# Kernel tuning notes

Hardware: AMD Instinct MI355X
Metric: run time of the kernel (lower is better)

## Reference

```python
import jax, jax.numpy as jnp
import numpy as np

DIM = 2048
NUM_HEADS = 16
HEAD_DIM = DIM // NUM_HEADS  # 128
LC = HEAD_DIM // 2           # 64 complex pairs per head
B, S = 2, 2048
EPS = 1e-6


def setup_inputs() -> dict:
    key = jax.random.key(0)
    ks = jax.random.split(key, 12)
    x = jax.random.normal(ks[0], (B, S, DIM), dtype=jnp.float32)
    # freqs: unit-modulus complex rotations stored as (cos, sin), shape [S,1,LC,2]
    theta = jax.random.uniform(ks[1], (S, 1, LC), dtype=jnp.float32) * (2.0 * np.pi)
    freqs = jnp.stack([jnp.cos(theta), jnp.sin(theta)], axis=-1)
    scale = 0.02
    wq = jax.random.normal(ks[2], (DIM, DIM), dtype=jnp.float32) * scale
    bq = jnp.zeros((DIM,), dtype=jnp.float32)
    wk = jax.random.normal(ks[3], (DIM, DIM), dtype=jnp.float32) * scale
    bk = jnp.zeros((DIM,), dtype=jnp.float32)
    wv = jax.random.normal(ks[4], (DIM, DIM), dtype=jnp.float32) * scale
    bv = jnp.zeros((DIM,), dtype=jnp.float32)
    wo = jax.random.normal(ks[5], (DIM, DIM), dtype=jnp.float32) * scale
    bo = jnp.zeros((DIM,), dtype=jnp.float32)
    gq = jnp.ones((DIM,), dtype=jnp.float32)   # RMSNorm weight for q
    gk = jnp.ones((DIM,), dtype=jnp.float32)   # RMSNorm weight for k
    return {"x": x, "freqs": freqs, "wq": wq, "bq": bq, "wk": wk, "bk": bk,
            "wv": wv, "bv": bv, "wo": wo, "bo": bo, "gq": gq, "gk": gk}


def _rms_norm(x, g):
    xf = x.astype(jnp.float32)
    y = xf * jax.lax.rsqrt(jnp.mean(xf * xf, axis=-1, keepdims=True) + EPS)
    return y.astype(x.dtype) * g


def _rope_apply(x, freqs):
    # x: [B,S,D] -> complex pairs [B,S,H,LC,2]; freqs: [S,1,LC,2] (cos,sin)
    b, s, _ = x.shape
    xp = x.astype(jnp.float32).reshape(b, s, NUM_HEADS, LC, 2)
    xr, xi = xp[..., 0], xp[..., 1]
    cr = freqs[None, :, :, :, 0]  # [1,S,1,LC]
    ci = freqs[None, :, :, :, 1]
    out_r = xr * cr - xi * ci
    out_i = xr * ci + xi * cr
    out = jnp.stack([out_r, out_i], axis=-1).reshape(b, s, DIM)
    return out.astype(x.dtype)


def _attention(q, k, v):
    # q,k,v: [B,S,D] -> multihead SDPA -> [B,S,D]
    b, s, _ = q.shape
    qh = q.reshape(b, s, NUM_HEADS, HEAD_DIM).transpose(0, 2, 1, 3)
    kh = k.reshape(b, s, NUM_HEADS, HEAD_DIM).transpose(0, 2, 1, 3)
    vh = v.reshape(b, s, NUM_HEADS, HEAD_DIM).transpose(0, 2, 1, 3)
    scale = 1.0 / np.sqrt(HEAD_DIM).astype(np.float32)
    scores = jnp.einsum('bhqd,bhkd->bhqk', qh, kh) * scale
    probs = jax.nn.softmax(scores, axis=-1)
    out = jnp.einsum('bhqk,bhkd->bhqd', probs, vh)
    return out.transpose(0, 2, 1, 3).reshape(b, s, DIM)


def reference(x, freqs, wq, bq, wk, bk, wv, bv, wo, bo, gq, gk):
    q = _rms_norm(x @ wq.T + bq, gq)
    k = _rms_norm(x @ wk.T + bk, gk)
    v = x @ wv.T + bv
    q = _rope_apply(q, freqs)
    k = _rope_apply(k, freqs)
    attn = _attention(q, k, v)
    return attn @ wo.T + bo
```

## Files before the change

### kernel.cpp

```cpp
#include <hip/hip_runtime.h>
#include <cstdint>

typedef __bf16 bf16;
typedef __bf16 bf16x8 __attribute__((ext_vector_type(8)));
typedef __bf16 bf16x4 __attribute__((ext_vector_type(4)));
typedef float f32x4 __attribute__((ext_vector_type(4)));

#define DIMN 2048
#define SEQ  2048
#define NH   16
#define HD   128

__device__ __forceinline__ void gld_lds16(const bf16* g, bf16* l) {
    __builtin_amdgcn_global_load_lds(
        (const __attribute__((address_space(1))) void*)g,
        (__attribute__((address_space(3))) void*)l,
        16, 0, 0);
}

__global__ __launch_bounds__(256) void cast_all(
    const float* __restrict__ x,
    const float* __restrict__ wq, const float* __restrict__ wk,
    const float* __restrict__ wv, const float* __restrict__ wo,
    bf16* __restrict__ xb,
    bf16* __restrict__ wqb, bf16* __restrict__ wkb,
    bf16* __restrict__ wvb, bf16* __restrict__ wob)
{
    int id = blockIdx.x;
    const float* src; bf16* dst; int i;
    if (id < 8192) { src = x; dst = xb; i = id * 256 + threadIdx.x; }
    else {
        id -= 8192;
        int w = id >> 12; id &= 4095;
        src = (w == 0) ? wq : (w == 1) ? wk : (w == 2) ? wv : wo;
        dst = (w == 0) ? wqb : (w == 1) ? wkb : (w == 2) ? wvb : wob;
        i = id * 256 + threadIdx.x;
    }
    float4 v = ((const float4*)src)[i];
    bf16x4 o;
    o[0] = (bf16)v.x; o[1] = (bf16)v.y; o[2] = (bf16)v.z; o[3] = (bf16)v.w;
    ((bf16x4*)dst)[i] = o;
}

template<int OUT_F32>
__global__ __launch_bounds__(256) void gemm_bt(
    const bf16* __restrict__ A,
    const bf16* __restrict__ Bw0, const bf16* __restrict__ Bw1, const bf16* __restrict__ Bw2,
    const float* __restrict__ bias0, const float* __restrict__ bias1, const float* __restrict__ bias2,
    void* __restrict__ C0, void* __restrict__ C1, void* __restrict__ C2)
{
    const int K = DIMN, N = DIMN;
    const int vtm = (!OUT_F32) && (blockIdx.z == 2);
    const bf16* Ap; const bf16* Bp; const float* bias; void* Cout;
    if (blockIdx.z == 0)      { Ap = A;   Bp = Bw0; bias = bias0; Cout = C0; }
    else if (blockIdx.z == 1) { Ap = A;   Bp = Bw1; bias = bias1; Cout = C1; }
    else                      { Ap = Bw2; Bp = A;   bias = bias2; Cout = C2; }

    __shared__ __attribute__((aligned(16))) bf16 As[128 * 64];
    __shared__ __attribute__((aligned(16))) bf16 Bs[128 * 64];

    const int t    = threadIdx.x;
    const int lane = t & 63, wave = t >> 6;
    const int l15  = lane & 15, quad = lane >> 4;
    const int wm   = (wave >> 1) * 64, wn = (wave & 1) * 64;
    const long bm = vtm ? (long)blockIdx.x * 128 : (long)blockIdx.y * 128;
    const long bn = vtm ? (long)blockIdx.y * 128 : (long)blockIdx.x * 128;

    const bf16* agp[4]; const bf16* bgp[4]; bf16* asd[4]; bf16* bsd[4];
#pragma unroll
    for (int it = 0; it < 4; it++) {
        int fs  = it * 256 + t;
        int row = fs >> 3;
        int gs  = (fs & 7) ^ (row & 7);
        agp[it] = Ap + (bm + row) * (long)K + gs * 8;
        bgp[it] = Bp + (bn + row) * (long)K + gs * 8;
        asd[it] = As + fs * 8;
        bsd[it] = Bs + fs * 8;
    }
    const int swl = l15 & 7;

    f32x4 acc[4][4] = {};

    for (int k0 = 0; k0 < K; k0 += 64) {
#pragma unroll
        for (int it = 0; it < 4; it++) {
            gld_lds16(agp[it] + k0, asd[it]);
            gld_lds16(bgp[it] + k0, bsd[it]);
        }
        __syncthreads();

#pragma unroll
        for (int ks2 = 0; ks2 < 2; ks2++) {
            const int sw = ((ks2 * 4 + quad) ^ swl) * 8;
            bf16x8 af[4], bfr[4];
#pragma unroll
            for (int i = 0; i < 4; i++)
                af[i] = *(const bf16x8*)(As + (wm + i * 16 + l15) * 64 + sw);
#pragma unroll
            for (int j = 0; j < 4; j++)
                bfr[j] = *(const bf16x8*)(Bs + (wn + j * 16 + l15) * 64 + sw);
#pragma unroll
            for (int i = 0; i < 4; i++)
#pragma unroll
                for (int j = 0; j < 4; j++)
                    acc[i][j] = __builtin_amdgcn_mfma_f32_16x16x32_bf16(af[i], bfr[j], acc[i][j], 0, 0, 0);
        }
        __syncthreads();
    }

    if (vtm) {
#pragma unroll
        for (int j = 0; j < 4; j++) {
            const long col = bn + wn + j * 16 + l15;
            const long cb = col >> 11, cs = col & (SEQ - 1);
#pragma unroll
            for (int i = 0; i < 4; i++) {
                const long m0 = bm + wm + i * 16 + quad * 4;
#pragma unroll
                for (int r = 0; r < 4; r++)
                    ((bf16*)Cout)[((cb * DIMN + m0 + r) * SEQ) + cs] =
                        (bf16)(acc[i][j][r] + bias[m0 + r]);
            }
        }
    } else {
#pragma unroll
        for (int j = 0; j < 4; j++) {
            const long col = bn + wn + j * 16 + l15;
            const float bv = bias[col];
#pragma unroll
            for (int i = 0; i < 4; i++) {
                const long row0 = bm + wm + i * 16 + quad * 4;
#pragma unroll
                for (int r = 0; r < 4; r++) {
                    float v = acc[i][j][r] + bv;
                    if (OUT_F32) ((float*)Cout)[(row0 + r) * N + col] = v;
                    else         ((bf16*)Cout)[(row0 + r) * N + col] = (bf16)v;
                }
            }
        }
    }
}

__global__ __launch_bounds__(256) void norm_prep(
    bf16* __restrict__ q, bf16* __restrict__ k,
    const float* __restrict__ gq, const float* __restrict__ gk,
    const float* __restrict__ freqs)
{
    const int id = blockIdx.x;
    const int t = threadIdx.x;
    const int qk  = id >> 12;
    const int row = id & 4095;
    bf16* ptr = qk ? k : q;
    const float* g = qk ? gk : gq;
    const float osc = qk ? 1.0f : 0.12753138080219222f;
    const int s = row & (SEQ - 1);
    const int lane = t & 63, wave = t >> 6;

    bf16* base = ptr + (long)row * DIMN + t * 8;
    bf16x8 raw = *(const bf16x8*)base;
    float v[8]; float ss = 0.f;
#pragma unroll
    for (int j = 0; j < 8; j++) { v[j] = (float)raw[j]; ss += v[j] * v[j]; }
#pragma unroll
    for (int off = 32; off; off >>= 1) ss += __shfl_xor(ss, off, 64);
    __shared__ float red[4];
    if (lane == 0) red[wave] = ss;
    __syncthreads();
    float tot = red[0] + red[1] + red[2] + red[3];
    float rn = rsqrtf(tot * (1.0f / DIMN) + 1e-6f);

    const int e0 = t * 8;
    bf16x8 o;
#pragma unroll
    for (int pp = 0; pp < 4; pp++) {
        int e = e0 + pp * 2;
        float xr = v[pp * 2]     * rn * g[e];
        float xi = v[pp * 2 + 1] * rn * g[e + 1];
        int lc = (e >> 1) & 63;
        float cr = freqs[s * 128 + lc * 2];
        float ci = freqs[s * 128 + lc * 2 + 1];
        o[pp * 2]     = (bf16)((xr * cr - xi * ci) * osc);
        o[pp * 2 + 1] = (bf16)((xr * ci + xi * cr) * osc);
    }
    *(bf16x8*)base = o;
}

__global__ __launch_bounds__(512, 2) void attention(
    const bf16* __restrict__ Q, const bf16* __restrict__ Kb,
    const bf16* __restrict__ Vt, bf16* __restrict__ O)
{
    __shared__ __attribute__((aligned(16))) bf16 Ksh[2][64 * 128];
    __shared__ __attribute__((aligned(16))) bf16 Vsh[2][128 * 64];
    __shared__ __attribute__((aligned(16))) bf16 Psh[8][32 * 72];
    __shared__ float Lsh[8][32];

    const int t = threadIdx.x;
    const int lane = t & 63, w = t >> 6;
    const int l15 = lane & 15, quad = lane >> 4;
    const int bh = blockIdx.x, b = bh >> 4, h = bh & 15;
    const int qt = blockIdx.y;
    const long qrow0 = (long)b * SEQ + qt * 256 + w * 32;
    const bf16* qbase = Q  + qrow0 * DIMN + h * HD;
    const bf16* kbase = Kb + (long)b * SEQ * DIMN + h * HD;
    const bf16* vbase = Vt + (long)bh * HD * SEQ;

    bf16x8 qf[2][4];
#pragma unroll
    for (int im = 0; im < 2; im++)
#pragma unroll
        for (int kd = 0; kd < 4; kd++)
            qf[im][kd] = *(const bf16x8*)(qbase + (long)(im * 16 + l15) * DIMN + kd * 32 + quad * 8);

    long koff[2], voff[2];
#pragma unroll
    for (int it = 0; it < 2; it++) {
        int fs = it * 512 + t;
        int kr = fs >> 4, kp = fs & 15;
        koff[it] = (long)kr * DIMN + (kp ^ (kr & 15)) * 8;
        int dr = fs >> 3, vp = fs & 7;
        voff[it] = (long)dr * SEQ + (vp ^ (dr & 7)) * 8;
    }

    f32x4 o_acc[2][8] = {};
    float Lt[2] = {0.f, 0.f};

#pragma unroll
    for (int it = 0; it < 2; it++) {
        gld_lds16(kbase + koff[it], &Ksh[0][(it * 512 + t) * 8]);
        gld_lds16(vbase + voff[it], &Vsh[0][(it * 512 + t) * 8]);
    }
    __syncthreads();

    for (int kt = 0; kt < 32; kt++) {
        const int cur = kt & 1;
        if (kt < 31) {
            const bf16* kg = kbase + (long)((kt + 1) * 64) * DIMN;
            const bf16* vg = vbase + (kt + 1) * 64;
#pragma unroll
            for (int it = 0; it < 2; it++) {
                gld_lds16(kg + koff[it], &Ksh[cur ^ 1][(it * 512 + t) * 8]);
                gld_lds16(vg + voff[it], &Vsh[cur ^ 1][(it * 512 + t) * 8]);
            }
        }
        const bf16* K0 = Ksh[cur];
        const bf16* V0 = Vsh[cur];

        f32x4 st[4][2] = {};
        __builtin_amdgcn_s_setprio(1);
#pragma unroll
        for (int jk = 0; jk < 4; jk++)
#pragma unroll
            for (int kd = 0; kd < 4; kd++) {
                bf16x8 kf = *(const bf16x8*)(K0 + (jk * 16 + l15) * 128 + (((kd * 4 + quad) ^ l15) & 15) * 8);
                st[jk][0] = __builtin_amdgcn_mfma_f32_16x16x32_bf16(kf, qf[0][kd], st[jk][0], 0, 0, 0);
                st[jk][1] = __builtin_amdgcn_mfma_f32_16x16x32_bf16(kf, qf[1][kd], st[jk][1], 0, 0, 0);
            }
        __builtin_amdgcn_s_setprio(0);

#pragma unroll
        for (int im = 0; im < 2; im++) {
            float part = 0.f;
#pragma unroll
            for (int jk = 0; jk < 4; jk++) {
                bf16x4 pk;
#pragma unroll
                for (int r = 0; r < 4; r++) {
                    float e = exp2f(st[jk][im][r]);
                    part += e;
                    pk[r] = (bf16)e;
                }
                *(bf16x4*)(Psh[w] + (im * 16 + l15) * 72 + jk * 16 + quad * 4) = pk;
            }
            Lt[im] += part;
        }

        __builtin_amdgcn_s_setprio(1);
#pragma unroll
        for (int kd2 = 0; kd2 < 2; kd2++) {
            bf16x8 pa[2];
            pa[0] = *(const bf16x8*)(Psh[w] + (l15)      * 72 + kd2 * 32 + quad * 8);
            pa[1] = *(const bf16x8*)(Psh[w] + (16 + l15) * 72 + kd2 * 32 + quad * 8);
#pragma unroll
            for (int dj = 0; dj < 8; dj++) {
                bf16x8 vfr = *(const bf16x8*)(V0 + (dj * 16 + l15) * 64 + (((kd2 * 4 + quad) ^ l15) & 7) * 8);
                o_acc[0][dj] = __builtin_amdgcn_mfma_f32_16x16x32_bf16(pa[0], vfr, o_acc[0][dj], 0, 0, 0);
                o_acc[1][dj] = __builtin_amdgcn_mfma_f32_16x16x32_bf16(pa[1], vfr, o_acc[1][dj], 0, 0, 0);
            }
        }
        __builtin_amdgcn_s_setprio(0);
        __syncthreads();
    }

#pragma unroll
    for (int im = 0; im < 2; im++) {
        Lt[im] += __shfl_xor(Lt[im], 16, 64);
        Lt[im] += __shfl_xor(Lt[im], 32, 64);
    }
    if (quad == 0) { Lsh[w][l15] = Lt[0]; Lsh[w][16 + l15] = Lt[1]; }
    __syncthreads();

#pragma unroll
    for (int im = 0; im < 2; im++)
#pragma unroll
        for (int r = 0; r < 4; r++) {
            float inv = 1.0f / Lsh[w][im * 16 + quad * 4 + r];
            long orow = qrow0 + im * 16 + quad * 4 + r;
#pragma unroll
            for (int dj = 0; dj < 8; dj++)
                O[orow * DIMN + h * HD + dj * 16 + l15] = (bf16)(o_acc[im][dj][r] * inv);
        }
}

extern "C" void kernel_launch(void* const* d_in, const int* in_sizes, int n_in,
                              void* d_out, int out_size, void* d_ws, size_t ws_size,
                              hipStream_t stream) {
    const float* x     = (const float*)d_in[0];
    const float* freqs = (const float*)d_in[1];
    const float* wq    = (const float*)d_in[2];
    const float* bq    = (const float*)d_in[3];
    const float* wk    = (const float*)d_in[4];
    const float* bk    = (const float*)d_in[5];
    const float* wv    = (const float*)d_in[6];
    const float* bv    = (const float*)d_in[7];
    const float* wo    = (const float*)d_in[8];
    const float* bo    = (const float*)d_in[9];
    const float* gq    = (const float*)d_in[10];
    const float* gk    = (const float*)d_in[11];
    float* out = (float*)d_out;

    const size_t MAT  = (size_t)4096 * 2048 * 2;
    const size_t WMAT = (size_t)2048 * 2048 * 2;
    char* p = (char*)d_ws;
    bf16* xb  = (bf16*)p; p += MAT;
    bf16* wqb = (bf16*)p; p += WMAT;
    bf16* wkb = (bf16*)p; p += WMAT;
    bf16* wvb = (bf16*)p; p += WMAT;
    bf16* wob = (bf16*)p; p += WMAT;
    bf16* qb  = (bf16*)p; p += MAT;
    bf16* kb  = (bf16*)p; p += MAT;
    bf16* vt  = (bf16*)p; p += MAT;
    bf16* attn = qb;

    cast_all<<<24576, 256, 0, stream>>>(x, wq, wk, wv, wo, xb, wqb, wkb, wvb, wob);

    gemm_bt<0><<<dim3(16, 32, 3), 256, 0, stream>>>(xb, wqb, wkb, wvb,
                                                    bq, bk, bv, qb, kb, vt);

    norm_prep<<<8192, 256, 0, stream>>>(qb, kb, gq, gk, freqs);
    attention<<<dim3(32, 8), 512, 0, stream>>>(qb, kb, vt, attn);
    gemm_bt<1><<<dim3(16, 32, 1), 256, 0, stream>>>(attn, wob, wob, wob,
                                                    bo, bo, bo, out, out, out);
}
```

Before: 401.9 us.

## Use 32x32 MFMA in attention with register-resident P via permlane swap

```diff
diff --git a/kernel.cpp b/kernel.cpp
--- a/kernel.cpp
+++ b/kernel.cpp
@@ -5,6 +5,7 @@
 typedef __bf16 bf16x8 __attribute__((ext_vector_type(8)));
 typedef __bf16 bf16x4 __attribute__((ext_vector_type(4)));
 typedef float f32x4 __attribute__((ext_vector_type(4)));
+typedef float f32x16 __attribute__((ext_vector_type(16)));
 
 #define DIMN 2048
 #define SEQ  2048
@@ -42,19 +43,12 @@
     ((bf16x4*)dst)[i] = o;
 }
 
-template<int OUT_F32>
+template<int OUT_F32, int VTM>
 __global__ __launch_bounds__(256) void gemm_bt(
-    const bf16* __restrict__ A,
-    const bf16* __restrict__ Bw0, const bf16* __restrict__ Bw1, const bf16* __restrict__ Bw2,
-    const float* __restrict__ bias0, const float* __restrict__ bias1, const float* __restrict__ bias2,
-    void* __restrict__ C0, void* __restrict__ C1, void* __restrict__ C2)
+    const bf16* __restrict__ A, const bf16* __restrict__ Bw,
+    const float* __restrict__ bias, void* __restrict__ Cout)
 {
     const int K = DIMN, N = DIMN;
-    const int vtm = (!OUT_F32) && (blockIdx.z == 2);
-    const bf16* Ap; const bf16* Bp; const float* bias; void* Cout;
-    if (blockIdx.z == 0)      { Ap = A;   Bp = Bw0; bias = bias0; Cout = C0; }
-    else if (blockIdx.z == 1) { Ap = A;   Bp = Bw1; bias = bias1; Cout = C1; }
-    else                      { Ap = Bw2; Bp = A;   bias = bias2; Cout = C2; }
 
     __shared__ __attribute__((aligned(16))) bf16 As[128 * 64];
     __shared__ __attribute__((aligned(16))) bf16 Bs[128 * 64];
@@ -63,8 +57,8 @@
     const int lane = t & 63, wave = t >> 6;
     const int l15  = lane & 15, quad = lane >> 4;
     const int wm   = (wave >> 1) * 64, wn = (wave & 1) * 64;
-    const long bm = vtm ? (long)blockIdx.x * 128 : (long)blockIdx.y * 128;
-    const long bn = vtm ? (long)blockIdx.y * 128 : (long)blockIdx.x * 128;
+    const long bm = VTM ? (long)blockIdx.x * 128 : (long)blockIdx.y * 128;
+    const long bn = VTM ? (long)blockIdx.y * 128 : (long)blockIdx.x * 128;
 
     const bf16* agp[4]; const bf16* bgp[4]; bf16* asd[4]; bf16* bsd[4];
 #pragma unroll
@@ -72,8 +66,8 @@
         int fs  = it * 256 + t;
         int row = fs >> 3;
         int gs  = (fs & 7) ^ (row & 7);
-        agp[it] = Ap + (bm + row) * (long)K + gs * 8;
-        bgp[it] = Bp + (bn + row) * (long)K + gs * 8;
+        agp[it] = A  + (bm + row) * (long)K + gs * 8;
+        bgp[it] = Bw + (bn + row) * (long)K + gs * 8;
         asd[it] = As + fs * 8;
         bsd[it] = Bs + fs * 8;
     }
@@ -108,7 +102,7 @@
         __syncthreads();
     }
 
-    if (vtm) {
+    if (VTM) {
 #pragma unroll
         for (int j = 0; j < 4; j++) {
             const long col = bn + wn + j * 16 + l15;
@@ -191,12 +185,10 @@
 {
     __shared__ __attribute__((aligned(16))) bf16 Ksh[2][64 * 128];
     __shared__ __attribute__((aligned(16))) bf16 Vsh[2][128 * 64];
-    __shared__ __attribute__((aligned(16))) bf16 Psh[8][32 * 72];
-    __shared__ float Lsh[8][32];
 
     const int t = threadIdx.x;
     const int lane = t & 63, w = t >> 6;
-    const int l15 = lane & 15, quad = lane >> 4;
+    const int l31 = lane & 31, hi = lane >> 5;
     const int bh = blockIdx.x, b = bh >> 4, h = bh & 15;
     const int qt = blockIdx.y;
     const long qrow0 = (long)b * SEQ + qt * 256 + w * 32;
@@ -204,12 +196,10 @@
     const bf16* kbase = Kb + (long)b * SEQ * DIMN + h * HD;
     const bf16* vbase = Vt + (long)bh * HD * SEQ;
 
-    bf16x8 qf[2][4];
-#pragma unroll
-    for (int im = 0; im < 2; im++)
-#pragma unroll
-        for (int kd = 0; kd < 4; kd++)
-            qf[im][kd] = *(const bf16x8*)(qbase + (long)(im * 16 + l15) * DIMN + kd * 32 + quad * 8);
+    bf16x8 qf[8];
+#pragma unroll
+    for (int kd = 0; kd < 8; kd++)
+        qf[kd] = *(const bf16x8*)(qbase + (long)l31 * DIMN + kd * 16 + hi * 8);
 
     long koff[2], voff[2];
 #pragma unroll
@@ -221,8 +211,8 @@
         voff[it] = (long)dr * SEQ + (vp ^ (dr & 7)) * 8;
     }
 
-    f32x4 o_acc[2][8] = {};
-    float Lt[2] = {0.f, 0.f};
+    f32x16 o_acc[4] = {};
+    float Lt = 0.f;
 
 #pragma unroll
     for (int it = 0; it < 2; it++) {
@@ -245,69 +235,75 @@
         const bf16* K0 = Ksh[cur];
         const bf16* V0 = Vsh[cur];
 
-        f32x4 st[4][2] = {};
+        f32x16 st0 = {}, st1 = {};
         __builtin_amdgcn_s_setprio(1);
 #pragma unroll
-        for (int jk = 0; jk < 4; jk++)
-#pragma unroll
-            for (int kd = 0; kd < 4; kd++) {
-                bf16x8 kf = *(const bf16x8*)(K0 + (jk * 16 + l15) * 128 + (((kd * 4 + quad) ^ l15) & 15) * 8);
-                st[jk][0] = __builtin_amdgcn_mfma_f32_16x16x32_bf16(kf, qf[0][kd], st[jk][0], 0, 0, 0);
-                st[jk][1] = __builtin_amdgcn_mfma_f32_16x16x32_bf16(kf, qf[1][kd], st[jk][1], 0, 0, 0);
-            }
+        for (int kd = 0; kd < 8; kd++) {
+            const int sg = ((kd * 2 + hi) ^ (lane & 15)) * 8;
+            bf16x8 kf0 = *(const bf16x8*)(K0 + (l31)      * 128 + sg);
+            bf16x8 kf1 = *(const bf16x8*)(K0 + (32 + l31) * 128 + sg);
+            st0 = __builtin_amdgcn_mfma_f32_32x32x16_bf16(kf0, qf[kd], st0, 0, 0, 0);
+            st1 = __builtin_amdgcn_mfma_f32_32x32x16_bf16(kf1, qf[kd], st1, 0, 0, 0);
+        }
         __builtin_amdgcn_s_setprio(0);
 
-#pragma unroll
-        for (int im = 0; im < 2; im++) {
-            float part = 0.f;
-#pragma unroll
-            for (int jk = 0; jk < 4; jk++) {
-                bf16x4 pk;
-#pragma unroll
-                for (int r = 0; r < 4; r++) {
-                    float e = exp2f(st[jk][im][r]);
-                    part += e;
-                    pk[r] = (bf16)e;
-                }
-                *(bf16x4*)(Psh[w] + (im * 16 + l15) * 72 + jk * 16 + quad * 4) = pk;
-            }
-            Lt[im] += part;
-        }
+        float part = 0.f;
+#pragma unroll
+        for (int r = 0; r < 16; r++) {
+            st0[r] = exp2f(st0[r]); part += st0[r];
+            st1[r] = exp2f(st1[r]); part += st1[r];
+        }
+        Lt += part;
 
         __builtin_amdgcn_s_setprio(1);
 #pragma unroll
-        for (int kd2 = 0; kd2 < 2; kd2++) {
-            bf16x8 pa[2];
-            pa[0] = *(const bf16x8*)(Psh[w] + (l15)      * 72 + kd2 * 32 + quad * 8);
-            pa[1] = *(const bf16x8*)(Psh[w] + (16 + l15) * 72 + kd2 * 32 + quad * 8);
-#pragma unroll
-            for (int dj = 0; dj < 8; dj++) {
-                bf16x8 vfr = *(const bf16x8*)(V0 + (dj * 16 + l15) * 64 + (((kd2 * 4 + quad) ^ l15) & 7) * 8);
-                o_acc[0][dj] = __builtin_amdgcn_mfma_f32_16x16x32_bf16(pa[0], vfr, o_acc[0][dj], 0, 0, 0);
-                o_acc[1][dj] = __builtin_amdgcn_mfma_f32_16x16x32_bf16(pa[1], vfr, o_acc[1][dj], 0, 0, 0);
+        for (int k = 0; k < 4; k++) {
+            const int base = 8 * (k & 1);
+            float e0, e1, e2, e3, e4, e5, e6, e7;
+            if (k < 2) {
+                e0 = st0[base]; e1 = st0[base+1]; e2 = st0[base+2]; e3 = st0[base+3];
+                e4 = st0[base+4]; e5 = st0[base+5]; e6 = st0[base+6]; e7 = st0[base+7];
+            } else {
+                e0 = st1[base]; e1 = st1[base+1]; e2 = st1[base+2]; e3 = st1[base+3];
+                e4 = st1[base+4]; e5 = st1[base+5]; e6 = st1[base+6]; e7 = st1[base+7];
+            }
+            uint32_t W0, W1, W2, W3;
+            asm("v_cvt_pk_bf16_f32 %0, %1, %2" : "=v"(W0) : "v"(e0), "v"(e1));
+            asm("v_cvt_pk_bf16_f32 %0, %1, %2" : "=v"(W1) : "v"(e2), "v"(e3));
+            asm("v_cvt_pk_bf16_f32 %0, %1, %2" : "=v"(W2) : "v"(e4), "v"(e5));
+            asm("v_cvt_pk_bf16_f32 %0, %1, %2" : "=v"(W3) : "v"(e6), "v"(e7));
+            asm volatile("v_permlane32_swap_b32 %0, %1" : "+v"(W0), "+v"(W2));
+            asm volatile("v_permlane32_swap_b32 %0, %1" : "+v"(W1), "+v"(W3));
+            union { uint32_t u[4]; bf16x8 v; } pu;
+            pu.u[0] = W0; pu.u[1] = W1; pu.u[2] = W2; pu.u[3] = W3;
+            const bf16x8 pa = pu.v;
+#pragma unroll
+            for (int dj = 0; dj < 4; dj++) {
+                const bf16x8 vfr = *(const bf16x8*)(V0 + (dj * 32 + l31) * 64 +
+                                                    (((2 * k + hi) ^ (lane & 7)) * 8));
+                o_acc[dj] = __builtin_amdgcn_mfma_f32_32x32x16_bf16(pa, vfr, o_acc[dj], 0, 0, 0);
             }
         }
         __builtin_amdgcn_s_setprio(0);
         __syncthreads();
     }
 
-#pragma unroll
-    for (int im = 0; im < 2; im++) {
-        Lt[im] += __shfl_xor(Lt[im], 16, 64);
-        Lt[im] += __shfl_xor(Lt[im], 32, 64);
-    }
-    if (quad == 0) { Lsh[w][l15] = Lt[0]; Lsh[w][16 + l15] = Lt[1]; }
-    __syncthreads();
-
-#pragma unroll
-    for (int im = 0; im < 2; im++)
-#pragma unroll
-        for (int r = 0; r < 4; r++) {
-            float inv = 1.0f / Lsh[w][im * 16 + quad * 4 + r];
-            long orow = qrow0 + im * 16 + quad * 4 + r;
-#pragma unroll
-            for (int dj = 0; dj < 8; dj++)
-                O[orow * DIMN + h * HD + dj * 16 + l15] = (bf16)(o_acc[im][dj][r] * inv);
+    float Lfull = Lt + __shfl_xor(Lt, 32, 64);
+
+    float inv_[16];
+#pragma unroll
+    for (int r = 0; r < 16; r++) {
+        int mr = (r & 3) + 8 * (r >> 2) + 4 * hi;
+        inv_[r] = 1.0f / __shfl(Lfull, mr, 64);
+    }
+
+#pragma unroll
+    for (int dj = 0; dj < 4; dj++)
+#pragma unroll
+        for (int r = 0; r < 16; r++) {
+            int mr = (r & 3) + 8 * (r >> 2) + 4 * hi;
+            long orow = qrow0 + mr;
+            O[orow * DIMN + h * HD + dj * 32 + l31] = (bf16)(o_acc[dj][r] * inv_[r]);
         }
 }
 
@@ -343,11 +339,11 @@
 
     cast_all<<<24576, 256, 0, stream>>>(x, wq, wk, wv, wo, xb, wqb, wkb, wvb, wob);
 
-    gemm_bt<0><<<dim3(16, 32, 3), 256, 0, stream>>>(xb, wqb, wkb, wvb,
-                                                    bq, bk, bv, qb, kb, vt);
+    gemm_bt<0, 0><<<dim3(16, 32), 256, 0, stream>>>(xb, wqb, bq, qb);
+    gemm_bt<0, 0><<<dim3(16, 32), 256, 0, stream>>>(xb, wkb, bk, kb);
+    gemm_bt<0, 1><<<dim3(16, 32), 256, 0, stream>>>(wvb, xb, bv, vt);
 
     norm_prep<<<8192, 256, 0, stream>>>(qb, kb, gq, gk, freqs);
     attention<<<dim3(32, 8), 512, 0, stream>>>(qb, kb, vt, attn);
-    gemm_bt<1><<<dim3(16, 32, 1), 256, 0, stream>>>(attn, wob, wob, wob,
-                                                    bo, bo, bo, out, out, out);
-}
+    gemm_bt<1, 0><<<dim3(16, 32), 256, 0, stream>>>(attn, wob, bo, out);
+}
```

New measurement: 405.4 us. No clear change (+0.9%).
